# Performance work log

Measured on AMD Instinct MI355X. Metric: run time of the kernel, lower is better.

## Reference

```python
import jax, jax.numpy as jnp
import numpy as np

DIM = 2048
N_HEADS = 16
HEAD_DIM = DIM // N_HEADS
ROPE_BASE = 10000.0


def rope_cos_sin(T, head_dim, dtype=jnp.float32):
    inv_freq = 1.0 / (ROPE_BASE ** (jnp.arange(0, head_dim, 2, dtype=jnp.float32) / head_dim))
    t = jnp.arange(T, dtype=jnp.float32)
    freqs = jnp.einsum('i,j->ij', t, inv_freq)          # [T, Hd/2]
    emb = jnp.concatenate([freqs, freqs], axis=-1)       # [T, Hd]
    return jnp.cos(emb).astype(dtype), jnp.sin(emb).astype(dtype)


def apply_rope(x, cos, sin):
    # x: [B,H,T,Hd]; cos/sin: [T,Hd]
    x1 = x[..., ::2]
    x2 = x[..., 1::2]
    # interleave (-x2, x1) back to [B,H,T,Hd]
    x_rot = jnp.stack([-x2, x1], axis=-1).reshape(x.shape)
    return x * cos[None, None, :, :] + x_rot * sin[None, None, :, :]


def setup_inputs() -> dict:
    key = jax.random.key(0)
    k1, k2, k3 = jax.random.split(key, 3)
    B, T = 2, 4096
    x = jax.random.normal(k1, (B, T, DIM), dtype=jnp.float32)
    w_qkv = jax.random.normal(k2, (3 * DIM, DIM), dtype=jnp.float32) * (1.0 / np.sqrt(DIM))
    w_proj = jax.random.normal(k3, (DIM, DIM), dtype=jnp.float32) * (1.0 / np.sqrt(DIM))
    return {"x": x, "w_qkv": w_qkv, "w_proj": w_proj}


def reference(x, w_qkv, w_proj):
    B, T, C = x.shape
    qkv = jnp.einsum('btc,dc->btd', x, w_qkv)            # [B,T,3C]
    q, k, v = jnp.split(qkv, 3, axis=-1)

    def split_heads(t):
        return t.reshape(B, T, N_HEADS, HEAD_DIM).transpose(0, 2, 1, 3)  # [B,H,T,Hd]

    q, k, v = split_heads(q), split_heads(k), split_heads(v)
    cos, sin = rope_cos_sin(T, HEAD_DIM, x.dtype)
    q = apply_rope(q, cos, sin)
    k = apply_rope(k, cos, sin)

    scale = 1.0 / np.sqrt(HEAD_DIM).astype(np.float32)
    att = jnp.einsum('bhqd,bhkd->bhqk', q, k) * scale     # [B,H,T,T]
    causal = jnp.tril(jnp.ones((T, T), dtype=bool))
    att = jnp.where(causal[None, None, :, :], att, jnp.finfo(att.dtype).min)
    att = jax.nn.softmax(att, axis=-1)
    out = jnp.einsum('bhqk,bhkd->bhqd', att, v)           # [B,H,T,Hd]
    out = out.transpose(0, 2, 1, 3).reshape(B, T, C)
    return jnp.einsum('btc,dc->btd', out, w_proj)
```

## Files before the change

kernel.cpp:

```cpp
#include <hip/hip_runtime.h>
#include <cstdint>
#include <cstddef>

#define B_SZ   2
#define T_SEQ  4096
#define DIM_   2048
#define NH_    16
#define HD_    128
#define QKVD   (3*DIM_)
#define SCALE_ 0.08838834764831845f
#define QSCALE_ 0.12751879524343564f
#define TAU_    8.0f

typedef __bf16 bf16x4 __attribute__((ext_vector_type(4)));
typedef __bf16 bf16x8 __attribute__((ext_vector_type(8)));
typedef float  f32x4  __attribute__((ext_vector_type(4)));

typedef const __attribute__((address_space(1))) void* gas_ptr_t;
typedef       __attribute__((address_space(3))) void* las_ptr_t;

#define GLOAD_LDS16(gp, lp) \
  __builtin_amdgcn_global_load_lds((gas_ptr_t)(gp), (las_ptr_t)(lp), 16, 0, 0)

#if defined(__has_builtin) && __has_builtin(__builtin_amdgcn_exp2f)
#define EXP2F(x) __builtin_amdgcn_exp2f(x)
#else
#define EXP2F(x) exp2f(x)
#endif

__global__ void cast_f32_bf16(const float* __restrict__ in,
                              __bf16* __restrict__ out, int n4) {
  int i = blockIdx.x * blockDim.x + threadIdx.x;
  if (i < n4) {
    float4 v = ((const float4*)in)[i];
    bf16x4 o = { (__bf16)v.x, (__bf16)v.y, (__bf16)v.z, (__bf16)v.w };
    ((bf16x4*)out)[i] = o;
  }
}

__device__ __forceinline__ void store_c(float* C, size_t idx, float v)  { C[idx] = v; }
__device__ __forceinline__ void store_c(__bf16* C, size_t idx, float v) { C[idx] = (__bf16)v; }

template <typename OutT>
__global__ __launch_bounds__(256, 2) void gemm_bt(const __bf16* __restrict__ A,
                                                  const __bf16* __restrict__ B,
                                                  OutT* __restrict__ C,
                                                  int M, int N, int K) {
  __shared__ __attribute__((aligned(16))) __bf16 As[128 * 32];
  __shared__ __attribute__((aligned(16))) __bf16 Bs[128 * 32];

  const int tid  = threadIdx.x;
  const int wave = tid >> 6;
  const int lane = tid & 63;
  const int lrow = lane & 15;
  const int quad = lane >> 4;
  const int m0 = blockIdx.x * 128;
  const int n0 = blockIdx.y * 128;
  const int wm = (wave & 1) * 64;
  const int wn = (wave >> 1) * 64;

  const __bf16* Ag = A + (size_t)(m0 + (tid >> 2)) * K + (tid & 3) * 8;
  const __bf16* Bg = B + (size_t)(n0 + (tid >> 2)) * K + (tid & 3) * 8;

  f32x4 acc[4][4] = {};

  for (int k0 = 0; k0 < K; k0 += 32) {
    __syncthreads();
    GLOAD_LDS16(Ag + k0,                 &As[wave * 16 * 32]);
    GLOAD_LDS16(Ag + k0 + (size_t)64*K,  &As[(64 + wave * 16) * 32]);
    GLOAD_LDS16(Bg + k0,                 &Bs[wave * 16 * 32]);
    GLOAD_LDS16(Bg + k0 + (size_t)64*K,  &Bs[(64 + wave * 16) * 32]);
    __syncthreads();

    bf16x8 a[4], b[4];
#pragma unroll
    for (int i = 0; i < 4; i++)
      a[i] = *(const bf16x8*)&As[(wm + i * 16 + lrow) * 32 + quad * 8];
#pragma unroll
    for (int j = 0; j < 4; j++)
      b[j] = *(const bf16x8*)&Bs[(wn + j * 16 + lrow) * 32 + quad * 8];
#pragma unroll
    for (int i = 0; i < 4; i++)
#pragma unroll
      for (int j = 0; j < 4; j++)
        acc[i][j] = __builtin_amdgcn_mfma_f32_16x16x32_bf16(a[i], b[j], acc[i][j], 0, 0, 0);
  }

#pragma unroll
  for (int i = 0; i < 4; i++)
#pragma unroll
    for (int j = 0; j < 4; j++)
#pragma unroll
      for (int r = 0; r < 4; r++) {
        size_t row = (size_t)(m0 + wm + i * 16 + quad * 4 + r);
        size_t col = (size_t)(n0 + wn + j * 16 + lrow);
        store_c(C, row * (size_t)N + col, acc[i][j][r]);
      }
}

__global__ void rope_split(const __bf16* __restrict__ qkv,
                           __bf16* __restrict__ Qo,
                           __bf16* __restrict__ Ko,
                           __bf16* __restrict__ Vt) {
  const long id  = (long)blockIdx.x * blockDim.x + threadIdx.x;
  const int row = (int)(id / 3072);
  const int p   = (int)(id % 3072);
  const int b = row >> 12;
  const int t = row & (T_SEQ - 1);
  const __bf16* src = qkv + (size_t)row * QKVD;

  if (p < 2048) {
    const bool isq = (p < 1024);
    const int pp = isq ? p : p - 1024;
    const int dp = pp * 2;
    const int h = dp >> 7, d = dp & 127;
    const int base = isq ? 0 : DIM_;
    const float x0 = (float)src[base + dp];
    const float x1 = (float)src[base + dp + 1];
    const int i0 = d & 63, i1 = (d + 1) & 63;
    const float kf = -0.20762050593049014f;
    float a0 = (float)t * exp2f(i0 * kf);
    float a1 = (float)t * exp2f(i1 * kf);
    float s0, c0, s1, c1;
    sincosf(a0, &s0, &c0);
    sincosf(a1, &s1, &c1);
    float y0 = x0 * c0 - x1 * s0;
    float y1 = x1 * c1 + x0 * s1;
    if (isq) { y0 *= QSCALE_; y1 *= QSCALE_; }
    __bf16* dst = (isq ? Qo : Ko) + (((size_t)(b * NH_ + h) * T_SEQ + t) * HD_ + d);
    dst[0] = (__bf16)y0;
    dst[1] = (__bf16)y1;
  } else {
    const int dp = (p - 2048) * 2;
    const int h = dp >> 7, d = dp & 127;
    __bf16 v0 = src[2 * DIM_ + dp];
    __bf16 v1 = src[2 * DIM_ + dp + 1];
    size_t base = (size_t)(b * NH_ + h) * HD_;
    Vt[(base + d)     * T_SEQ + t] = v0;
    Vt[(base + d + 1) * T_SEQ + t] = v1;
  }
}

__global__ __launch_bounds__(512, 2) void flash_attn(const __bf16* __restrict__ Q,
                                                     const __bf16* __restrict__ K,
                                                     const __bf16* __restrict__ Vt,
                                                     __bf16* __restrict__ O) {
  __shared__ __attribute__((aligned(16))) __bf16 Ks[2][64 * 128];
  __shared__ __attribute__((aligned(16))) __bf16 Vs[2][128 * 64];
  __shared__ __attribute__((aligned(16))) __bf16 Ps[8][32 * 64];

  const int qb   = (gridDim.x - 1) - blockIdx.x;
  const int bh   = blockIdx.y;
  const int tid  = threadIdx.x;
  const int wave = tid >> 6;
  const int lane = tid & 63;
  const int l15  = lane & 15;
  const int quad = lane >> 4;

  const __bf16* Qh = Q  + (size_t)bh * T_SEQ * HD_;
  const __bf16* Kh = K  + (size_t)bh * T_SEQ * HD_;
  const __bf16* Vh = Vt + (size_t)bh * HD_ * T_SEQ;

  const int qw   = qb * 256 + wave * 32;
  const int kcnt = 4 * qb + 4;

  bf16x8 qf[2][4];
#pragma unroll
  for (int qt = 0; qt < 2; qt++)
#pragma unroll
    for (int kc = 0; kc < 4; kc++)
      qf[qt][kc] = *(const bf16x8*)&Qh[(size_t)(qw + qt * 16 + l15) * HD_ + kc * 32 + quad * 8];

  f32x4 o[2][8] = {};
  float m_[2] = {-1e30f, -1e30f};
  float l_[2] = {0.f, 0.f};

  const int krow = tid >> 3, kq8 = tid & 7;
  const int vrow = tid >> 2, vh4 = tid & 3;

  bf16x8 kpre[2], vpre[2];

#define LOAD_TILES(KB)                                                          \
  {                                                                             \
    const __bf16* kg = Kh + (size_t)((KB) * 64 + krow) * HD_;                   \
    const __bf16* vg = Vh + (size_t)vrow * T_SEQ + (KB) * 64;                   \
    _Pragma("unroll")                                                           \
    for (int j = 0; j < 2; j++) {                                               \
      kpre[j] = *(const bf16x8*)&kg[(j * 8 + kq8) * 8];                         \
      vpre[j] = *(const bf16x8*)&vg[(vh4 * 2 + j) * 8];                         \
    }                                                                           \
  }

#define STORE_TILES(BUF)                                                        \
  {                                                                             \
    _Pragma("unroll")                                                           \
    for (int j = 0; j < 2; j++) {                                               \
      int kc_ = (j * 8 + kq8) ^ (krow & 7);                                     \
      *(bf16x8*)&Ks[BUF][krow * 128 + kc_ * 8] = kpre[j];                       \
      int vc_ = (vh4 * 2 + j) ^ (vrow & 7);                                     \
      *(bf16x8*)&Vs[BUF][vrow * 64 + vc_ * 8] = vpre[j];                        \
    }                                                                           \
  }

  LOAD_TILES(0);
  STORE_TILES(0);
  if (kcnt > 1) LOAD_TILES(1);
  __syncthreads();

  for (int kb = 0; kb < kcnt; ++kb) {
    const int cur = kb & 1;
    if (kb + 1 < kcnt) STORE_TILES((kb + 1) & 1);
    if (kb + 2 < kcnt) LOAD_TILES(kb + 2);

    if (kb * 64 <= qw + 31) {
      f32x4 st[2][4];
#pragma unroll
      for (int kt = 0; kt < 4; kt++) {
        f32x4 a0 = {}, a1 = {};
        const int row = kt * 16 + l15;
#pragma unroll
        for (int kc = 0; kc < 4; kc++) {
          const int c = kc * 4 + quad;
          bf16x8 kf = *(const bf16x8*)&Ks[cur][row * 128 + (c ^ (row & 7)) * 8];
          a0 = __builtin_amdgcn_mfma_f32_16x16x32_bf16(kf, qf[0][kc], a0, 0, 0, 0);
          a1 = __builtin_amdgcn_mfma_f32_16x16x32_bf16(kf, qf[1][kc], a1, 0, 0, 0);
        }
        st[0][kt] = a0; st[1][kt] = a1;
      }

      if (kb * 64 + 63 > qw) {
#pragma unroll
        for (int qt = 0; qt < 2; qt++)
#pragma unroll
          for (int kt = 0; kt < 4; kt++)
#pragma unroll
            for (int r = 0; r < 4; r++) {
              int key = kb * 64 + kt * 16 + quad * 4 + r;
              int q   = qw + qt * 16 + l15;
              if (key > q) st[qt][kt][r] = -1e30f;
            }
      }

      float alpha[2];
      bool  needr[2];
#pragma unroll
      for (int qt = 0; qt < 2; qt++) {
        float mt = -1e30f;
#pragma unroll
        for (int kt = 0; kt < 4; kt++)
#pragma unroll
          for (int r = 0; r < 4; r++) mt = fmaxf(mt, st[qt][kt][r]);
        mt = fmaxf(mt, __shfl_xor(mt, 16));
        mt = fmaxf(mt, __shfl_xor(mt, 32));

        const bool need = __any(mt > m_[qt] + TAU_) != 0;
        needr[qt] = need;
        float mnew;
        if (need) {
          mnew = fmaxf(m_[qt], mt);
          alpha[qt] = EXP2F(m_[qt] - mnew);
          m_[qt] = mnew;
        } else {
          mnew = m_[qt];
          alpha[qt] = 1.0f;
        }

        float ps = 0.f;
        const int prow = qt * 16 + l15;
#pragma unroll
        for (int kt = 0; kt < 4; kt++) {
          bf16x4 pk;
#pragma unroll
          for (int r = 0; r < 4; r++) {
            float pv = EXP2F(st[qt][kt][r] - mnew);
            ps += pv;
            pk[r] = (__bf16)pv;
          }
          const int ec = kt * 16 + quad * 4;
          const int c  = (ec >> 3) ^ (prow & 7);
          *(bf16x4*)&Ps[wave][prow * 64 + c * 8 + (ec & 7)] = pk;
        }
        ps += __shfl_xor(ps, 16);
        ps += __shfl_xor(ps, 32);
        l_[qt] = l_[qt] * alpha[qt] + ps;
      }

      __asm__ volatile("s_waitcnt lgkmcnt(0)" ::: "memory");

#pragma unroll
      for (int qt = 0; qt < 2; qt++)
        if (needr[qt]) {
#pragma unroll
          for (int r = 0; r < 4; r++) {
            float a = __shfl(alpha[qt], quad * 4 + r);
#pragma unroll
            for (int dt = 0; dt < 8; dt++) o[qt][dt][r] *= a;
          }
        }

#pragma unroll
      for (int kc2 = 0; kc2 < 2; kc2++) {
        const int ec = kc2 * 32 + quad * 8;
        const int pc = (ec >> 3) ^ (l15 & 7);
        bf16x8 pf0 = *(const bf16x8*)&Ps[wave][(l15)      * 64 + pc * 8];
        bf16x8 pf1 = *(const bf16x8*)&Ps[wave][(16 + l15) * 64 + pc * 8];
#pragma unroll
        for (int dt = 0; dt < 8; dt++) {
          const int vr = dt * 16 + l15;
          const int vc = (ec >> 3) ^ (vr & 7);
          bf16x8 vf = *(const bf16x8*)&Vs[cur][vr * 64 + vc * 8];
          o[0][dt] = __builtin_amdgcn_mfma_f32_16x16x32_bf16(pf0, vf, o[0][dt], 0, 0, 0);
          o[1][dt] = __builtin_amdgcn_mfma_f32_16x16x32_bf16(pf1, vf, o[1][dt], 0, 0, 0);
        }
      }
    }
    __syncthreads();
  }

  const int b = bh >> 4, h = bh & 15;
#pragma unroll
  for (int qt = 0; qt < 2; qt++) {
    float il = 1.f / l_[qt];
#pragma unroll
    for (int r = 0; r < 4; r++) {
      float linv = __shfl(il, quad * 4 + r);
      int t = qw + qt * 16 + quad * 4 + r;
#pragma unroll
      for (int dt = 0; dt < 8; dt++) {
        size_t idx = (((size_t)b * T_SEQ + t) * NH_ + h) * HD_ + dt * 16 + l15;
        O[idx] = (__bf16)(o[qt][dt][r] * linv);
      }
    }
  }
}

extern "C" void kernel_launch(void* const* d_in, const int* in_sizes, int n_in,
                              void* d_out, int out_size, void* d_ws, size_t ws_size,
                              hipStream_t stream) {
  const float* x      = (const float*)d_in[0];
  const float* w_qkv  = (const float*)d_in[1];
  const float* w_proj = (const float*)d_in[2];
  float* out = (float*)d_out;

  char* ws = (char*)d_ws;
  const size_t SZ_X16   = (size_t)B_SZ * T_SEQ * DIM_ * 2;
  const size_t SZ_W16   = (size_t)QKVD * DIM_ * 2;
  const size_t SZ_WP16  = (size_t)DIM_ * DIM_ * 2;
  const size_t SZ_QKV16 = (size_t)B_SZ * T_SEQ * QKVD * 2;
  const size_t SZ_HEADS = SZ_X16;

  __bf16* x16   = (__bf16*)(ws);
  __bf16* w16   = (__bf16*)(ws + SZ_X16);
  __bf16* wp16  = (__bf16*)(ws + SZ_X16 + SZ_W16);
  __bf16* qkv16 = (__bf16*)(ws + SZ_X16 + SZ_W16 + SZ_WP16);
  __bf16* K16   = (__bf16*)(ws + SZ_X16 + SZ_W16 + SZ_WP16 + SZ_QKV16);
  __bf16* Vt16  = (__bf16*)(ws + SZ_X16 + SZ_W16 + SZ_WP16 + SZ_QKV16 + SZ_HEADS);
  __bf16* Q16   = x16;
  __bf16* O16   = qkv16;

  const size_t NEED = SZ_X16 + SZ_W16 + SZ_WP16 + SZ_QKV16 + 2 * SZ_HEADS;
  if (ws_size < NEED) return;

  {
    int n4 = (int)((size_t)B_SZ * T_SEQ * DIM_ / 4);
    cast_f32_bf16<<<(n4 + 255) / 256, 256, 0, stream>>>(x, x16, n4);
    n4 = (int)((size_t)QKVD * DIM_ / 4);
    cast_f32_bf16<<<(n4 + 255) / 256, 256, 0, stream>>>(w_qkv, w16, n4);
    n4 = (int)((size_t)DIM_ * DIM_ / 4);
    cast_f32_bf16<<<(n4 + 255) / 256, 256, 0, stream>>>(w_proj, wp16, n4);
  }

  gemm_bt<__bf16><<<dim3(8192 / 128, QKVD / 128), 256, 0, stream>>>(
      x16, w16, qkv16, 8192, QKVD, DIM_);

  {
    long total = (long)B_SZ * T_SEQ * 3072;
    rope_split<<<(int)(total / 256), 256, 0, stream>>>(qkv16, Q16, K16, Vt16);
  }

  flash_attn<<<dim3(T_SEQ / 256, B_SZ * NH_), 512, 0, stream>>>(Q16, K16, Vt16, O16);

  gemm_bt<float><<<dim3(8192 / 128, DIM_ / 128), 256, 0, stream>>>(
      O16, wp16, out, 8192, DIM_, DIM_);
}
```

Baseline: 868.5 us.

## Halve P staging buffer and process query tiles sequentially for higher occupancy

Each wave now writes its softmax probabilities to LDS one 16-row query tile at a time and runs the PV MFMAs for that tile before moving to the next. This halves the per-wave P staging buffer and cuts the kernel's LDS footprint so that more blocks can share a CU. The launch bound rises from 2 to 4 blocks, which forces a much tighter register budget. The risks are register spilling, V fragments being read from LDS twice (once per query tile), and extra LDS wait barriers that reduce instruction-level parallelism.

```diff
diff --git a/kernel.cpp b/kernel.cpp
--- a/kernel.cpp
+++ b/kernel.cpp
@@ -141,13 +141,13 @@
   }
 }
 
-__global__ __launch_bounds__(512, 2) void flash_attn(const __bf16* __restrict__ Q,
+__global__ __launch_bounds__(512, 4) void flash_attn(const __bf16* __restrict__ Q,
                                                      const __bf16* __restrict__ K,
                                                      const __bf16* __restrict__ Vt,
                                                      __bf16* __restrict__ O) {
   __shared__ __attribute__((aligned(16))) __bf16 Ks[2][64 * 128];
   __shared__ __attribute__((aligned(16))) __bf16 Vs[2][128 * 64];
-  __shared__ __attribute__((aligned(16))) __bf16 Ps[8][32 * 64];
+  __shared__ __attribute__((aligned(16))) __bf16 Ps[8][16 * 64];
 
   const int qb   = (gridDim.x - 1) - blockIdx.x;
   const int bh   = blockIdx.y;
@@ -241,8 +241,6 @@
             }
       }
 
-      float alpha[2];
-      bool  needr[2];
 #pragma unroll
       for (int qt = 0; qt < 2; qt++) {
         float mt = -1e30f;
@@ -254,63 +252,60 @@
         mt = fmaxf(mt, __shfl_xor(mt, 32));
 
         const bool need = __any(mt > m_[qt] + TAU_) != 0;
-        needr[qt] = need;
-        float mnew;
+        float mnew, alpha;
         if (need) {
           mnew = fmaxf(m_[qt], mt);
-          alpha[qt] = EXP2F(m_[qt] - mnew);
+          alpha = EXP2F(m_[qt] - mnew);
           m_[qt] = mnew;
         } else {
           mnew = m_[qt];
-          alpha[qt] = 1.0f;
+          alpha = 1.0f;
         }
 
         float ps = 0.f;
-        const int prow = qt * 16 + l15;
-#pragma unroll
-        for (int kt = 0; kt < 4; kt++) {
-          bf16x4 pk;
+        bf16x4 pk[4];
+#pragma unroll
+        for (int kt = 0; kt < 4; kt++)
 #pragma unroll
           for (int r = 0; r < 4; r++) {
             float pv = EXP2F(st[qt][kt][r] - mnew);
             ps += pv;
-            pk[r] = (__bf16)pv;
+            pk[kt][r] = (__bf16)pv;
           }
-          const int ec = kt * 16 + quad * 4;
-          const int c  = (ec >> 3) ^ (prow & 7);
-          *(bf16x4*)&Ps[wave][prow * 64 + c * 8 + (ec & 7)] = pk;
-        }
         ps += __shfl_xor(ps, 16);
         ps += __shfl_xor(ps, 32);
-        l_[qt] = l_[qt] * alpha[qt] + ps;
-      }
-
-      __asm__ volatile("s_waitcnt lgkmcnt(0)" ::: "memory");
-
-#pragma unroll
-      for (int qt = 0; qt < 2; qt++)
-        if (needr[qt]) {
+        l_[qt] = l_[qt] * alpha + ps;
+
+        __asm__ volatile("s_waitcnt lgkmcnt(0)" ::: "memory");
+#pragma unroll
+        for (int kt = 0; kt < 4; kt++) {
+          const int ec = kt * 16 + quad * 4;
+          const int c  = (ec >> 3) ^ (l15 & 7);
+          *(bf16x4*)&Ps[wave][l15 * 64 + c * 8 + (ec & 7)] = pk[kt];
+        }
+        __asm__ volatile("s_waitcnt lgkmcnt(0)" ::: "memory");
+
+        if (need) {
 #pragma unroll
           for (int r = 0; r < 4; r++) {
-            float a = __shfl(alpha[qt], quad * 4 + r);
+            float a = __shfl(alpha, quad * 4 + r);
 #pragma unroll
             for (int dt = 0; dt < 8; dt++) o[qt][dt][r] *= a;
           }
         }
 
 #pragma unroll
-      for (int kc2 = 0; kc2 < 2; kc2++) {
-        const int ec = kc2 * 32 + quad * 8;
-        const int pc = (ec >> 3) ^ (l15 & 7);
-        bf16x8 pf0 = *(const bf16x8*)&Ps[wave][(l15)      * 64 + pc * 8];
-        bf16x8 pf1 = *(const bf16x8*)&Ps[wave][(16 + l15) * 64 + pc * 8];
-#pragma unroll
-        for (int dt = 0; dt < 8; dt++) {
-          const int vr = dt * 16 + l15;
-          const int vc = (ec >> 3) ^ (vr & 7);
-          bf16x8 vf = *(const bf16x8*)&Vs[cur][vr * 64 + vc * 8];
-          o[0][dt] = __builtin_amdgcn_mfma_f32_16x16x32_bf16(pf0, vf, o[0][dt], 0, 0, 0);
-          o[1][dt] = __builtin_amdgcn_mfma_f32_16x16x32_bf16(pf1, vf, o[1][dt], 0, 0, 0);
+        for (int kc2 = 0; kc2 < 2; kc2++) {
+          const int ec = kc2 * 32 + quad * 8;
+          const int pc = (ec >> 3) ^ (l15 & 7);
+          bf16x8 pf = *(const bf16x8*)&Ps[wave][l15 * 64 + pc * 8];
+#pragma unroll
+          for (int dt = 0; dt < 8; dt++) {
+            const int vr = dt * 16 + l15;
+            const int vc = (ec >> 3) ^ (vr & 7);
+            bf16x8 vf = *(const bf16x8*)&Vs[cur][vr * 64 + vc * 8];
+            o[qt][dt] = __builtin_amdgcn_mfma_f32_16x16x32_bf16(pf, vf, o[qt][dt], 0, 0, 0);
+          }
         }
       }
     }
```

New measurement: 1.833 ms. 111% more time.
